# Performance work log

Hardware: AMD Instinct MI355X
Metric: run time of the kernel (lower is better)

## Reference

```python
import jax, jax.numpy as jnp
import numpy as np

N_NODES = 50000
HIDDEN = 128
N_REL = 9
N_LAYERS = 3
N_EDGES = 600000


def setup_inputs() -> dict:
    key = jax.random.key(0)
    k1, k2, k3, k4, k5 = jax.random.split(key, 5)
    edge_index = jax.random.randint(k1, (2, N_EDGES), 0, N_NODES, dtype=jnp.int64 if jax.config.jax_enable_x64 else jnp.int32)
    edge_type = jax.random.randint(k2, (N_EDGES,), 0, N_REL, dtype=edge_index.dtype)
    embeddings = jax.random.uniform(k3, (N_NODES, HIDDEN), dtype=jnp.float32)
    weights = jax.random.uniform(k4, (N_LAYERS, N_REL, HIDDEN, HIDDEN), dtype=jnp.float32)
    biases = jax.random.uniform(k5, (N_LAYERS, N_REL, HIDDEN), dtype=jnp.float32)
    return {"edge_index": edge_index, "edge_type": edge_type,
            "embeddings": embeddings, "weights": weights, "biases": biases}


def reference(edge_index, edge_type, embeddings, weights, biases):
    # RGCN: per relation r, messages = emb[src] @ W[l,r] + b[l,r], scatter-summed
    # into dest. Equivalent vectorized form: precompute X = emb @ W for all
    # relations ([R,N,E]), then a single gather + segment_sum over edges.
    L = weights.shape[0]
    N = embeddings.shape[0]
    dest = edge_index[0]
    src = edge_index[1]
    out = embeddings
    for l in range(L):
        X = jnp.einsum('ne,ref->rnf', out, weights[l])        # [R, N, E]
        msg = X[edge_type, src] + biases[l][edge_type]        # [num_edges, E]
        hidden = jax.ops.segment_sum(msg, dest, num_segments=N)  # [N, E]
        if l + 1 < L:
            hidden = jax.nn.relu(hidden)
        out = hidden
    return out
```

## Files before the change

### kernel.cpp

```cpp
#include <hip/hip_runtime.h>

#define NNODES 50000
#define HID 128
#define NREL 9
#define NLAYERS 3
#define NEDGES 600000

#define NBINS (NREL * NNODES)
#define SCAN_CHUNK 1024
#define NBLK ((NBINS + SCAN_CHUNK - 1) / SCAN_CHUNK)

#define KTOT (NREL * HID)
#define GM2 64
#define FPITCH 136

typedef __attribute__((ext_vector_type(8))) short short8;
typedef __attribute__((ext_vector_type(4))) float f32x4;

__device__ __forceinline__ short f2bf(float f) {
    union { float f; unsigned u; } c; c.f = f;
    unsigned r = c.u + 0x7fff + ((c.u >> 16) & 1);
    return (short)(r >> 16);
}
__device__ __forceinline__ float bf2f(short v) {
    return __uint_as_float(((unsigned)(unsigned short)v) << 16);
}


__global__ void hist2_kernel(const int* __restrict__ dst, const int* __restrict__ etype,
                             int* __restrict__ bins) {
    int e = blockIdx.x * blockDim.x + threadIdx.x;
    if (e < NEDGES) {
        int bin = etype[e] * NNODES + dst[e];
        atomicAdd(&bins[bin], 1);
    }
}

__global__ __launch_bounds__(256) void scan_pass1(const int* __restrict__ bins,
                                                  int* __restrict__ blocksum) {
    __shared__ int red[256];
    int b = blockIdx.x, t = threadIdx.x;
    int i0 = b * SCAN_CHUNK + t * 4;
    int s = 0;
#pragma unroll
    for (int k = 0; k < 4; k++)
        if (i0 + k < NBINS) s += bins[i0 + k];
    red[t] = s;
    __syncthreads();
    for (int off = 128; off > 0; off >>= 1) {
        if (t < off) red[t] += red[t + off];
        __syncthreads();
    }
    if (t == 0) blocksum[b] = red[0];
}

__global__ __launch_bounds__(512) void scan_pass2(const int* __restrict__ blocksum,
                                                  int* __restrict__ blockoff,
                                                  int* __restrict__ rowptr) {
    __shared__ int s[512];
    int t = threadIdx.x;
    int v = (t < NBLK) ? blocksum[t] : 0;
    s[t] = v;
    __syncthreads();
    for (int off = 1; off < 512; off <<= 1) {
        int x = (t >= off) ? s[t - off] : 0;
        __syncthreads();
        s[t] += x;
        __syncthreads();
    }
    if (t < NBLK) blockoff[t] = s[t] - v;
    if (t == 0) rowptr[NBINS] = NEDGES;
}

__global__ __launch_bounds__(256) void scan_pass3(const int* __restrict__ bins,
                                                  const int* __restrict__ blockoff,
                                                  int* __restrict__ rowptr,
                                                  int* __restrict__ cursor) {
    __shared__ int sc[256];
    int b = blockIdx.x, t = threadIdx.x;
    int i0 = b * SCAN_CHUNK + t * 4;
    int v[4], p[4];
    int s = 0;
#pragma unroll
    for (int k = 0; k < 4; k++) {
        v[k] = (i0 + k < NBINS) ? bins[i0 + k] : 0;
        p[k] = s;
        s += v[k];
    }
    sc[t] = s;
    __syncthreads();
    for (int off = 1; off < 256; off <<= 1) {
        int x = (t >= off) ? sc[t - off] : 0;
        __syncthreads();
        sc[t] += x;
        __syncthreads();
    }
    int base = blockoff[b] + (sc[t] - s);
#pragma unroll
    for (int k = 0; k < 4; k++) {
        if (i0 + k < NBINS) {
            rowptr[i0 + k] = base + p[k];
            cursor[i0 + k] = base + p[k];
        }
    }
}

__global__ void place_kernel(const int* __restrict__ dst, const int* __restrict__ src,
                             const int* __restrict__ etype,
                             int* __restrict__ cursor, int* __restrict__ bsrc) {
    int e = blockIdx.x * blockDim.x + threadIdx.x;
    if (e < NEDGES) {
        int bin = etype[e] * NNODES + dst[e];
        int pos = atomicAdd(&cursor[bin], 1);
        bsrc[pos] = src[e];
    }
}


__global__ __launch_bounds__(256) void convert_w(const float* __restrict__ W,
                                                 short* __restrict__ Wt2) {
    int lr = blockIdx.x;
    int l = lr / NREL, r = lr - l * NREL;
    const float* w = W + (size_t)lr * HID * HID;
    short* o = Wt2 + (size_t)l * HID * KTOT;
    int tid = threadIdx.x;
#pragma unroll 4
    for (int i = 0; i < 64; i++) {
        int elem = i * 256 + tid;
        int kk = elem >> 7, n = elem & 127;
        o[(size_t)n * KTOT + r * HID + kk] = f2bf(w[elem]);
    }
}

__global__ __launch_bounds__(256) void convert_emb(const float* __restrict__ E,
                                                   short* __restrict__ Ebf) {
    int gid = blockIdx.x * blockDim.x + threadIdx.x;
    const float* p = E + (size_t)gid * 8;
    float4 v0 = *(const float4*)p;
    float4 v1 = *(const float4*)(p + 4);
    short8 o = {f2bf(v0.x), f2bf(v0.y), f2bf(v0.z), f2bf(v0.w),
                f2bf(v1.x), f2bf(v1.y), f2bf(v1.z), f2bf(v1.w)};
    *(short8*)(Ebf + (size_t)gid * 8) = o;
}


__global__ __launch_bounds__(256) void fused_kernel(const short* __restrict__ Hin,
                                                    const short* __restrict__ Wt2l,
                                                    const float* __restrict__ Bias,
                                                    const int* __restrict__ rowptr,
                                                    const int* __restrict__ bsrc,
                                                    short* __restrict__ HoutBf,
                                                    float* __restrict__ HoutF,
                                                    int last) {
    __shared__ short As[GM2 * FPITCH];
    __shared__ int   rp_s[NREL * (GM2 + 1)];
    __shared__ float bias_s[NREL * HID];

    int tid  = threadIdx.x;
    int wave = tid >> 6, lane = tid & 63;
    int lm = lane & 15, lq = lane >> 4;
    int row0 = blockIdx.x * GM2;
    int n0   = wave * 32;

    for (int i = tid; i < NREL * (GM2 + 1); i += 256) {
        int r = i / (GM2 + 1), o = i - r * (GM2 + 1);
        int d = row0 + o; if (d > NNODES) d = NNODES;
        rp_s[i] = rowptr[r * NNODES + d];
    }
    for (int i = tid; i < NREL * HID; i += 256) bias_s[i] = Bias[i];

    int grow = tid >> 2;
    int gcc  = tid & 3;

    f32x4 acc[4][2];
#pragma unroll
    for (int a = 0; a < 4; a++)
#pragma unroll
        for (int b = 0; b < 2; b++) acc[a][b] = (f32x4){0.f, 0.f, 0.f, 0.f};

    __syncthreads();

    const short* wb = Wt2l + (size_t)(n0 + lm) * KTOT + lq * 8;

    for (int r = 0; r < NREL; r++) {
        int rs = rp_s[r * (GM2 + 1) + grow];
        int re = rp_s[r * (GM2 + 1) + grow + 1];
        float ga[32];
#pragma unroll
        for (int i = 0; i < 32; i++) ga[i] = 0.f;
        int j = rs;
        while (j + 1 < re) {
            int s0 = bsrc[j];
            int s1 = bsrc[j + 1];
            const short8* h0 = (const short8*)(Hin + (size_t)s0 * HID + gcc * 32);
            const short8* h1 = (const short8*)(Hin + (size_t)s1 * HID + gcc * 32);
            short8 a0 = h0[0], a1 = h0[1], a2 = h0[2], a3 = h0[3];
            short8 b0 = h1[0], b1 = h1[1], b2 = h1[2], b3 = h1[3];
#pragma unroll
            for (int i = 0; i < 8; i++) {
                ga[i]      += bf2f(a0[i]) + bf2f(b0[i]);
                ga[i + 8]  += bf2f(a1[i]) + bf2f(b1[i]);
                ga[i + 16] += bf2f(a2[i]) + bf2f(b2[i]);
                ga[i + 24] += bf2f(a3[i]) + bf2f(b3[i]);
            }
            j += 2;
        }
        if (j < re) {
            int s0 = bsrc[j];
            const short8* h0 = (const short8*)(Hin + (size_t)s0 * HID + gcc * 32);
            short8 a0 = h0[0], a1 = h0[1], a2 = h0[2], a3 = h0[3];
#pragma unroll
            for (int i = 0; i < 8; i++) {
                ga[i]      += bf2f(a0[i]);
                ga[i + 8]  += bf2f(a1[i]);
                ga[i + 16] += bf2f(a2[i]);
                ga[i + 24] += bf2f(a3[i]);
            }
        }

        __syncthreads();
        {
            short8 o0, o1, o2, o3;
#pragma unroll
            for (int i = 0; i < 8; i++) {
                o0[i] = f2bf(ga[i]);
                o1[i] = f2bf(ga[i + 8]);
                o2[i] = f2bf(ga[i + 16]);
                o3[i] = f2bf(ga[i + 24]);
            }
            short8* ap = (short8*)&As[grow * FPITCH + gcc * 32];
            ap[0] = o0; ap[1] = o1; ap[2] = o2; ap[3] = o3;
        }
        __syncthreads();

#pragma unroll
        for (int ks = 0; ks < 4; ks++) {
            short8 af[4];
#pragma unroll
            for (int mt = 0; mt < 4; mt++)
                af[mt] = *(const short8*)&As[(mt * 16 + lm) * FPITCH + ks * 32 + lq * 8];
#pragma unroll
            for (int nt = 0; nt < 2; nt++) {
                short8 bf = *(const short8*)(wb + (size_t)nt * 16 * KTOT + r * HID + ks * 32);
                __builtin_amdgcn_s_setprio(1);
#pragma unroll
                for (int mt = 0; mt < 4; mt++)
                    acc[mt][nt] = __builtin_amdgcn_mfma_f32_16x16x32_bf16(af[mt], bf, acc[mt][nt], 0, 0, 0);
                __builtin_amdgcn_s_setprio(0);
            }
        }
    }

    __syncthreads();

    if (!last) {
        short (*Et)[FPITCH] = (short(*)[FPITCH])As;
#pragma unroll
        for (int mt = 0; mt < 4; mt++) {
#pragma unroll
            for (int reg = 0; reg < 4; reg++) {
                int rl = mt * 16 + lq * 4 + reg;
                float cr[NREL];
#pragma unroll
                for (int rr = 0; rr < NREL; rr++)
                    cr[rr] = (float)(rp_s[rr * (GM2 + 1) + rl + 1] - rp_s[rr * (GM2 + 1) + rl]);
#pragma unroll
                for (int nt = 0; nt < 2; nt++) {
                    int n = n0 + nt * 16 + lm;
                    float b = 0.f;
#pragma unroll
                    for (int rr = 0; rr < NREL; rr++) b += cr[rr] * bias_s[rr * HID + n];
                    float o = fmaxf(acc[mt][nt][reg] + b, 0.f);
                    Et[rl][n] = f2bf(o);
                }
            }
        }
        __syncthreads();
#pragma unroll
        for (int i = 0; i < 4; i++) {
            int p = i * 256 + tid;
            int row = p >> 4, cc = p & 15;
            int d = row0 + row;
            if (d < NNODES)
                *(short8*)(HoutBf + (size_t)d * HID + cc * 8) = *(const short8*)&Et[row][cc * 8];
        }
    } else {
#pragma unroll
        for (int mt = 0; mt < 4; mt++) {
#pragma unroll
            for (int reg = 0; reg < 4; reg++) {
                int rl = mt * 16 + lq * 4 + reg;
                int d  = row0 + rl;
                if (d >= NNODES) continue;
                float cr[NREL];
#pragma unroll
                for (int rr = 0; rr < NREL; rr++)
                    cr[rr] = (float)(rp_s[rr * (GM2 + 1) + rl + 1] - rp_s[rr * (GM2 + 1) + rl]);
#pragma unroll
                for (int nt = 0; nt < 2; nt++) {
                    int n = n0 + nt * 16 + lm;
                    float b = 0.f;
#pragma unroll
                    for (int rr = 0; rr < NREL; rr++) b += cr[rr] * bias_s[rr * HID + n];
                    HoutF[(size_t)d * HID + n] = acc[mt][nt][reg] + b;
                }
            }
        }
    }
}


extern "C" void kernel_launch(void* const* d_in, const int* in_sizes, int n_in,
                              void* d_out, int out_size, void* d_ws, size_t ws_size,
                              hipStream_t stream) {
    const int*   edge_index = (const int*)d_in[0];
    const int*   etype      = (const int*)d_in[1];
    const float* emb        = (const float*)d_in[2];
    const float* W          = (const float*)d_in[3];
    const float* Bias       = (const float*)d_in[4];
    float*       out        = (float*)d_out;

    const int* dst  = edge_index;
    const int* srcA = edge_index + NEDGES;

    short* Ebf  = (short*)d_ws;
    short* HbfA = Ebf  + (size_t)NNODES * HID;
    short* HbfB = HbfA + (size_t)NNODES * HID;
    short* Wt2  = HbfB + (size_t)NNODES * HID;
    int*   bsrc     = (int*)(Wt2 + (size_t)NLAYERS * HID * KTOT);
    int*   bins     = bsrc + NEDGES;
    int*   cursor   = bins + NBINS;
    int*   rowptr   = cursor + NBINS;
    int*   blocksum = rowptr + NBINS + 1;
    int*   blockoff = blocksum + NBLK;

    hipMemsetAsync(bins, 0, NBINS * sizeof(int), stream);
    hist2_kernel<<<(NEDGES + 255) / 256, 256, 0, stream>>>(dst, etype, bins);
    scan_pass1<<<NBLK, 256, 0, stream>>>(bins, blocksum);
    scan_pass2<<<1, 512, 0, stream>>>(blocksum, blockoff, rowptr);
    scan_pass3<<<NBLK, 256, 0, stream>>>(bins, blockoff, rowptr, cursor);
    place_kernel<<<(NEDGES + 255) / 256, 256, 0, stream>>>(dst, srcA, etype, cursor, bsrc);
    convert_w<<<NLAYERS * NREL, 256, 0, stream>>>(W, Wt2);
    convert_emb<<<(NNODES * HID / 8) / 256, 256, 0, stream>>>(emb, Ebf);

    const int nblocks = (NNODES + GM2 - 1) / GM2;
    const short* Hin = Ebf;
    for (int l = 0; l < NLAYERS; l++) {
        int last = (l + 1 == NLAYERS);
        short* Hout = (l == 0) ? HbfA : HbfB;
        if (l == 2) Hout = HbfA;
        const short* Wtl = Wt2 + (size_t)l * HID * KTOT;
        const float* Bl  = Bias + (size_t)l * NREL * HID;
        fused_kernel<<<nblocks, 256, 0, stream>>>(
            Hin, Wtl, Bl, rowptr, bsrc, Hout, out, last);
        Hin = Hout;
    }
}
```

Measured before the change: 510.8 us.

## Halve fused-kernel row tile and double-buffer the gather tile in LDS

Shrinks the per-block node tile from 64 to 32 rows, giving twice as many blocks, and splits each row's gather across 8 threads instead of 4 to cut the per-thread accumulator registers. The LDS A-tile is double-buffered by relation parity, which removes one barrier per relation, and weight fragments are loaded into registers before the gather. Launch bounds now request 4 blocks per CU to raise occupancy and hide the latency of the irregular gather. The cost is that each weight fragment is reused by fewer MFMA rows, so weight traffic per node doubles, and the bias and rowptr setup is repeated across more blocks.

```diff
diff --git a/kernel.cpp b/kernel.cpp
--- a/kernel.cpp
+++ b/kernel.cpp
@@ -11,7 +11,7 @@
 #define NBLK ((NBINS + SCAN_CHUNK - 1) / SCAN_CHUNK)
 
 #define KTOT (NREL * HID)
-#define GM2 64
+#define GM2 32
 #define FPITCH 136
 
 typedef __attribute__((ext_vector_type(8))) short short8;
@@ -144,15 +144,15 @@
 }
 
 
-__global__ __launch_bounds__(256) void fused_kernel(const short* __restrict__ Hin,
-                                                    const short* __restrict__ Wt2l,
-                                                    const float* __restrict__ Bias,
-                                                    const int* __restrict__ rowptr,
-                                                    const int* __restrict__ bsrc,
-                                                    short* __restrict__ HoutBf,
-                                                    float* __restrict__ HoutF,
-                                                    int last) {
-    __shared__ short As[GM2 * FPITCH];
+__global__ __launch_bounds__(256, 4) void fused_kernel(const short* __restrict__ Hin,
+                                                       const short* __restrict__ Wt2l,
+                                                       const float* __restrict__ Bias,
+                                                       const int* __restrict__ rowptr,
+                                                       const int* __restrict__ bsrc,
+                                                       short* __restrict__ HoutBf,
+                                                       float* __restrict__ HoutF,
+                                                       int last) {
+    __shared__ short As[2][GM2 * FPITCH];
     __shared__ int   rp_s[NREL * (GM2 + 1)];
     __shared__ float bias_s[NREL * HID];
 
@@ -169,12 +169,13 @@
     }
     for (int i = tid; i < NREL * HID; i += 256) bias_s[i] = Bias[i];
 
-    int grow = tid >> 2;
+    int grow = tid >> 3;
     int gcc  = tid & 3;
-
-    f32x4 acc[4][2];
-#pragma unroll
-    for (int a = 0; a < 4; a++)
+    gcc = tid & 7;
+
+    f32x4 acc[2][2];
+#pragma unroll
+    for (int a = 0; a < 2; a++)
 #pragma unroll
         for (int b = 0; b < 2; b++) acc[a][b] = (f32x4){0.f, 0.f, 0.f, 0.f};
 
@@ -183,80 +184,77 @@
     const short* wb = Wt2l + (size_t)(n0 + lm) * KTOT + lq * 8;
 
     for (int r = 0; r < NREL; r++) {
+        short* Ap = &As[r & 1][0];
+
+        short8 bfr[2][4];
+#pragma unroll
+        for (int nt = 0; nt < 2; nt++)
+#pragma unroll
+            for (int ks = 0; ks < 4; ks++)
+                bfr[nt][ks] = *(const short8*)(wb + (size_t)nt * 16 * KTOT + r * HID + ks * 32);
+
         int rs = rp_s[r * (GM2 + 1) + grow];
         int re = rp_s[r * (GM2 + 1) + grow + 1];
-        float ga[32];
-#pragma unroll
-        for (int i = 0; i < 32; i++) ga[i] = 0.f;
+        float ga[16];
+#pragma unroll
+        for (int i = 0; i < 16; i++) ga[i] = 0.f;
         int j = rs;
         while (j + 1 < re) {
             int s0 = bsrc[j];
             int s1 = bsrc[j + 1];
-            const short8* h0 = (const short8*)(Hin + (size_t)s0 * HID + gcc * 32);
-            const short8* h1 = (const short8*)(Hin + (size_t)s1 * HID + gcc * 32);
-            short8 a0 = h0[0], a1 = h0[1], a2 = h0[2], a3 = h0[3];
-            short8 b0 = h1[0], b1 = h1[1], b2 = h1[2], b3 = h1[3];
+            const short8* h0 = (const short8*)(Hin + (size_t)s0 * HID + gcc * 16);
+            const short8* h1 = (const short8*)(Hin + (size_t)s1 * HID + gcc * 16);
+            short8 a0 = h0[0], a1 = h0[1];
+            short8 b0 = h1[0], b1 = h1[1];
 #pragma unroll
             for (int i = 0; i < 8; i++) {
-                ga[i]      += bf2f(a0[i]) + bf2f(b0[i]);
-                ga[i + 8]  += bf2f(a1[i]) + bf2f(b1[i]);
-                ga[i + 16] += bf2f(a2[i]) + bf2f(b2[i]);
-                ga[i + 24] += bf2f(a3[i]) + bf2f(b3[i]);
+                ga[i]     += bf2f(a0[i]) + bf2f(b0[i]);
+                ga[i + 8] += bf2f(a1[i]) + bf2f(b1[i]);
             }
             j += 2;
         }
         if (j < re) {
             int s0 = bsrc[j];
-            const short8* h0 = (const short8*)(Hin + (size_t)s0 * HID + gcc * 32);
-            short8 a0 = h0[0], a1 = h0[1], a2 = h0[2], a3 = h0[3];
+            const short8* h0 = (const short8*)(Hin + (size_t)s0 * HID + gcc * 16);
+            short8 a0 = h0[0], a1 = h0[1];
 #pragma unroll
             for (int i = 0; i < 8; i++) {
-                ga[i]      += bf2f(a0[i]);
-                ga[i + 8]  += bf2f(a1[i]);
-                ga[i + 16] += bf2f(a2[i]);
-                ga[i + 24] += bf2f(a3[i]);
-            }
-        }
-
-        __syncthreads();
+                ga[i]     += bf2f(a0[i]);
+                ga[i + 8] += bf2f(a1[i]);
+            }
+        }
+
         {
-            short8 o0, o1, o2, o3;
+            short8 o0, o1;
 #pragma unroll
             for (int i = 0; i < 8; i++) {
                 o0[i] = f2bf(ga[i]);
                 o1[i] = f2bf(ga[i + 8]);
-                o2[i] = f2bf(ga[i + 16]);
-                o3[i] = f2bf(ga[i + 24]);
-            }
-            short8* ap = (short8*)&As[grow * FPITCH + gcc * 32];
-            ap[0] = o0; ap[1] = o1; ap[2] = o2; ap[3] = o3;
+            }
+            short8* ap = (short8*)&Ap[grow * FPITCH + gcc * 16];
+            ap[0] = o0; ap[1] = o1;
         }
         __syncthreads();
 
 #pragma unroll
         for (int ks = 0; ks < 4; ks++) {
-            short8 af[4];
-#pragma unroll
-            for (int mt = 0; mt < 4; mt++)
-                af[mt] = *(const short8*)&As[(mt * 16 + lm) * FPITCH + ks * 32 + lq * 8];
-#pragma unroll
-            for (int nt = 0; nt < 2; nt++) {
-                short8 bf = *(const short8*)(wb + (size_t)nt * 16 * KTOT + r * HID + ks * 32);
-                __builtin_amdgcn_s_setprio(1);
-#pragma unroll
-                for (int mt = 0; mt < 4; mt++)
-                    acc[mt][nt] = __builtin_amdgcn_mfma_f32_16x16x32_bf16(af[mt], bf, acc[mt][nt], 0, 0, 0);
-                __builtin_amdgcn_s_setprio(0);
-            }
+            short8 af0 = *(const short8*)&Ap[(lm     ) * FPITCH + ks * 32 + lq * 8];
+            short8 af1 = *(const short8*)&Ap[(lm + 16) * FPITCH + ks * 32 + lq * 8];
+            __builtin_amdgcn_s_setprio(1);
+            acc[0][0] = __builtin_amdgcn_mfma_f32_16x16x32_bf16(af0, bfr[0][ks], acc[0][0], 0, 0, 0);
+            acc[1][0] = __builtin_amdgcn_mfma_f32_16x16x32_bf16(af1, bfr[0][ks], acc[1][0], 0, 0, 0);
+            acc[0][1] = __builtin_amdgcn_mfma_f32_16x16x32_bf16(af0, bfr[1][ks], acc[0][1], 0, 0, 0);
+            acc[1][1] = __builtin_amdgcn_mfma_f32_16x16x32_bf16(af1, bfr[1][ks], acc[1][1], 0, 0, 0);
+            __builtin_amdgcn_s_setprio(0);
         }
     }
 
     __syncthreads();
 
     if (!last) {
-        short (*Et)[FPITCH] = (short(*)[FPITCH])As;
-#pragma unroll
-        for (int mt = 0; mt < 4; mt++) {
+        short (*Et)[FPITCH] = (short(*)[FPITCH])&As[0][0];
+#pragma unroll
+        for (int mt = 0; mt < 2; mt++) {
 #pragma unroll
             for (int reg = 0; reg < 4; reg++) {
                 int rl = mt * 16 + lq * 4 + reg;
@@ -277,7 +275,7 @@
         }
         __syncthreads();
 #pragma unroll
-        for (int i = 0; i < 4; i++) {
+        for (int i = 0; i < 2; i++) {
             int p = i * 256 + tid;
             int row = p >> 4, cc = p & 15;
             int d = row0 + row;
@@ -286,7 +284,7 @@
         }
     } else {
 #pragma unroll
-        for (int mt = 0; mt < 4; mt++) {
+        for (int mt = 0; mt < 2; mt++) {
 #pragma unroll
             for (int reg = 0; reg < 4; reg++) {
                 int rl = mt * 16 + lq * 4 + reg;
```

Result: faster. 471.2 us (-7.8%).
